# Kernel tuning notes

Hardware: AMD Instinct MI355X
Metric: run time of the kernel (lower is better)

Reference implementation:

```python
import jax, jax.numpy as jnp
import numpy as np

B, NQ, D, NH, L, P = 8, 1000, 256, 8, 4, 4
DFF = 1024
HD = D // NH
SHAPES = np.array([[128, 128], [64, 64], [32, 32], [16, 16]], dtype=np.int64)
S = int((SHAPES[:, 0] * SHAPES[:, 1]).sum())  # 21760
LEVEL_START = np.concatenate([np.zeros(1, np.int64), np.cumsum(SHAPES[:, 0] * SHAPES[:, 1])[:-1]])


def setup_inputs() -> dict:
    key = jax.random.key(0)
    ks = jax.random.split(key, 20)
    w = lambda k, shape, s=0.02: jax.random.normal(k, shape, jnp.float32) * s
    z = lambda n: jnp.zeros((n,), jnp.float32)
    return dict(
        query=w(ks[0], (B, NQ, D), 1.0),
        query_pos=w(ks[1], (B, NQ, D), 1.0),
        reference_points=jax.random.uniform(ks[2], (B, NQ, L, 4), jnp.float32),
        input_flatten=w(ks[3], (B, S, D), 1.0),
        input_spatial_shapes=SHAPES,
        input_level_start_index=LEVEL_START,
        Wq=w(ks[4], (D, D)), bq=z(D), Wk=w(ks[5], (D, D)), bk=z(D),
        Wv=w(ks[6], (D, D)), bv=z(D), Wo=w(ks[7], (D, D)), bo=z(D),
        ln1_g=jnp.ones((D,), jnp.float32), ln1_b=z(D),
        W_off=w(ks[8], (D, NH * L * P * 2)), b_off=z(NH * L * P * 2),
        W_attn=w(ks[9], (D, NH * L * P)), b_attn=z(NH * L * P),
        W_val=w(ks[10], (D, D)), b_val=z(D),
        W_cout=w(ks[11], (D, D)), b_cout=z(D),
        ln2_g=jnp.ones((D,), jnp.float32), ln2_b=z(D),
        W1=w(ks[12], (D, DFF)), b1=z(DFF),
        W2=w(ks[13], (DFF, D)), b2=z(D),
        ln3_g=jnp.ones((D,), jnp.float32), ln3_b=z(D),
    )


def layer_norm(x, g, b, eps=1e-5):
    mu = x.mean(-1, keepdims=True)
    var = ((x - mu) ** 2).mean(-1, keepdims=True)
    return (x - mu) / jnp.sqrt(var + eps) * g + b


def _ms_deform(value, shapes_np, loc, aw):
    # value: (B,S,NH,HD); loc: (B,Nq,NH,L,P,2) in [0,1]; aw: (B,Nq,NH,L,P)
    Bz, _, nh, hd = value.shape
    Nq = loc.shape[1]
    awt = aw.transpose(0, 2, 1, 3, 4)  # (B,NH,Nq,L,P)
    acc = jnp.zeros((Bz, nh, Nq, hd), value.dtype)
    start = 0
    for lvl in range(shapes_np.shape[0]):
        Hl, Wl = int(shapes_np[lvl, 0]), int(shapes_np[lvl, 1])
        vf = value[:, start:start + Hl * Wl].transpose(0, 2, 1, 3)  # (B,NH,Hl*Wl,HD)
        start += Hl * Wl
        # grid_sample align_corners=False: pixel coord = loc * size - 0.5
        lx = loc[:, :, :, lvl, :, 0].transpose(0, 2, 1, 3) * Wl - 0.5  # (B,NH,Nq,P)
        ly = loc[:, :, :, lvl, :, 1].transpose(0, 2, 1, 3) * Hl - 0.5
        x0 = jnp.floor(lx); y0 = jnp.floor(ly)
        tx = lx - x0; ty = ly - y0
        x0i = x0.astype(jnp.int32); y0i = y0.astype(jnp.int32)

        def gather(xi, yi):
            valid = (xi >= 0) & (xi < Wl) & (yi >= 0) & (yi < Hl)
            idx = jnp.clip(yi, 0, Hl - 1) * Wl + jnp.clip(xi, 0, Wl - 1)
            out = jnp.take_along_axis(vf, idx.reshape(Bz, nh, Nq * P)[..., None], axis=2)
            return out.reshape(Bz, nh, Nq, P, hd) * valid[..., None]

        g00 = gather(x0i, y0i)
        g01 = gather(x0i + 1, y0i)
        g10 = gather(x0i, y0i + 1)
        g11 = gather(x0i + 1, y0i + 1)
        samp = (g00 * ((1 - tx) * (1 - ty))[..., None] + g01 * (tx * (1 - ty))[..., None]
                + g10 * ((1 - tx) * ty)[..., None] + g11 * (tx * ty)[..., None])  # (B,NH,Nq,P,HD)
        acc = acc + jnp.einsum('bhqp,bhqpd->bhqd', awt[:, :, :, lvl], samp)
    return acc.transpose(0, 2, 1, 3).reshape(Bz, Nq, nh * hd)


def reference(query, query_pos, reference_points, input_flatten, input_spatial_shapes,
              input_level_start_index, Wq, bq, Wk, bk, Wv, bv, Wo, bo, ln1_g, ln1_b,
              W_off, b_off, W_attn, b_attn, W_val, b_val, W_cout, b_cout, ln2_g, ln2_b,
              W1, b1, W2, b2, ln3_g, ln3_b):
    Bz, Nq, Dm = query.shape
    # --- self-attention (post-norm), pos added to Q/K only ---
    qp = query + query_pos
    q = (qp @ Wq + bq).reshape(Bz, Nq, NH, HD)
    k = (qp @ Wk + bk).reshape(Bz, Nq, NH, HD)
    v = (query @ Wv + bv).reshape(Bz, Nq, NH, HD)
    att = jax.nn.softmax(jnp.einsum('bqhd,bkhd->bhqk', q, k) / jnp.sqrt(jnp.float32(HD)), axis=-1)
    sa = jnp.einsum('bhqk,bkhd->bqhd', att, v).reshape(Bz, Nq, Dm) @ Wo + bo
    x = layer_norm(query + sa, ln1_g, ln1_b)
    # --- deformable cross-attention ---
    q2 = x + query_pos
    value = (input_flatten @ W_val + b_val).reshape(Bz, -1, NH, HD)
    off = (q2 @ W_off + b_off).reshape(Bz, Nq, NH, L, P, 2)
    aw = jax.nn.softmax((q2 @ W_attn + b_attn).reshape(Bz, Nq, NH, L * P), axis=-1)
    aw = aw.reshape(Bz, Nq, NH, L, P)
    rp = reference_points  # (B,Nq,L,4) cxcywh
    loc = rp[:, :, None, :, None, :2] + off / P * rp[:, :, None, :, None, 2:] * 0.5
    shapes_np = np.asarray(input_spatial_shapes)
    ca = _ms_deform(value, shapes_np, loc, aw) @ W_cout + b_cout
    x = layer_norm(x + ca, ln2_g, ln2_b)
    # --- FFN ---
    ffn = jax.nn.relu(x @ W1 + b1) @ W2 + b2
    return layer_norm(x + ffn, ln3_g, ln3_b)
```

## Files before the change

kernel.cpp:

```cpp
#include <hip/hip_runtime.h>
#include <hip/hip_bf16.h>

#define B_   8
#define NQ_  1000
#define D_   256
#define NH_  8
#define L_   4
#define P_   4
#define DFF_ 1024
#define HD_  32
#define S_   21760
#define NTOK (B_*NQ_)

typedef short  bf16x8 __attribute__((ext_vector_type(8)));
typedef float  f32x4  __attribute__((ext_vector_type(4)));

#define WAITBAR(N) asm volatile("s_waitcnt vmcnt(" #N ") lgkmcnt(0)\n\ts_barrier" ::: "memory")
#define ENDBAR()   asm volatile("s_barrier" ::: "memory")

__device__ inline unsigned short f32_to_bf16_bits(float f) {
    unsigned int u = __float_as_uint(f);
    unsigned int rounding = 0x7FFFu + ((u >> 16) & 1u);
    u += rounding;
    return (unsigned short)(u >> 16);
}
__device__ inline float bf16_bits_to_f32(unsigned short b) {
    return __uint_as_float(((unsigned int)b) << 16);
}
__device__ inline unsigned int pack_trunc(float f0, float f1) {
    return __builtin_amdgcn_perm(__float_as_uint(f1), __float_as_uint(f0), 0x07060302u);
}
__device__ inline void async_copy16(const void* g, void* l) {
    __builtin_amdgcn_global_load_lds((const __attribute__((address_space(1))) unsigned int*)g,
                                     (__attribute__((address_space(3))) unsigned int*)l, 16, 0, 0);
}

struct PrepArgs {
    const float* wsrc[10];
    unsigned short* wdst[10];
    int wK[10], wN[10];
    const float* bq; const float* bk; const float* bv; const float* boff; const float* battn;
    float* qkvb; float* oab;
    const float* query; const float* qpos;
    unsigned short* q_bf; unsigned short* qp_bf;
};
__global__ __launch_bounds__(256) void prep_k(PrepArgs P)
{
    const int bid = blockIdx.x, tid = threadIdx.x;
    if (bid < 640) {
        const int job = bid >> 6, tile = bid & 63;
        const int K = P.wK[job], N = P.wN[job];
        const int tilesN = N >> 6;
        if (tile >= (K >> 6) * tilesN) return;
        const int kt = tile / tilesN, nt = tile - kt * tilesN;
        const int k0 = kt * 64, n0 = nt * 64;
        __shared__ unsigned short t_[64][65];
        const float* src = P.wsrc[job];
        unsigned short* dst = P.wdst[job];
        const int cc = tid & 63, rr = tid >> 6;
        #pragma unroll
        for (int i = 0; i < 16; i++) {
            int k = i * 4 + rr;
            t_[k][cc] = f32_to_bf16_bits(src[(size_t)(k0 + k) * N + n0 + cc]);
        }
        __syncthreads();
        #pragma unroll
        for (int i = 0; i < 16; i++) {
            int n = i * 4 + rr;
            dst[(size_t)(n0 + n) * K + k0 + cc] = t_[cc][n];
        }
    } else if (bid == 640) {
        P.qkvb[tid]       = P.bq[tid];
        P.qkvb[256 + tid] = P.bk[tid];
        P.qkvb[512 + tid] = P.bv[tid];
        P.oab[tid]        = P.boff[tid];
        if (tid < 128) P.oab[256 + tid] = P.battn[tid];
    } else {
        const int base = (bid - 641) * 1024 + tid;
        float4 fq[4][2], fp[4][2];
        #pragma unroll
        for (int i = 0; i < 4; i++) {
            const float* q = P.query + (size_t)(base + i * 256) * 8;
            const float* p = P.qpos  + (size_t)(base + i * 256) * 8;
            fq[i][0] = *reinterpret_cast<const float4*>(q);
            fq[i][1] = *reinterpret_cast<const float4*>(q + 4);
            fp[i][0] = *reinterpret_cast<const float4*>(p);
            fp[i][1] = *reinterpret_cast<const float4*>(p + 4);
        }
        #pragma unroll
        for (int i = 0; i < 4; i++) {
            uint4 tq, tp;
            tq.x = pack_trunc(fq[i][0].x, fq[i][0].y);
            tq.y = pack_trunc(fq[i][0].z, fq[i][0].w);
            tq.z = pack_trunc(fq[i][1].x, fq[i][1].y);
            tq.w = pack_trunc(fq[i][1].z, fq[i][1].w);
            tp.x = pack_trunc(fq[i][0].x + fp[i][0].x, fq[i][0].y + fp[i][0].y);
            tp.y = pack_trunc(fq[i][0].z + fp[i][0].z, fq[i][0].w + fp[i][0].w);
            tp.z = pack_trunc(fq[i][1].x + fp[i][1].x, fq[i][1].y + fp[i][1].y);
            tp.w = pack_trunc(fq[i][1].z + fp[i][1].z, fq[i][1].w + fp[i][1].w);
            *reinterpret_cast<uint4*>(P.q_bf  + (size_t)(base + i * 256) * 8) = tq;
            *reinterpret_cast<uint4*>(P.qp_bf + (size_t)(base + i * 256) * 8) = tp;
        }
    }
}

__global__ __launch_bounds__(256) void vgemmF(const float* __restrict__ Af,
                                              const unsigned short* __restrict__ Bt,
                                              const float* __restrict__ bias,
                                              unsigned short* __restrict__ Cb)
{
    constexpr int K = 256;
    constexpr int N = 256;
    __shared__ __align__(16) float          sA[2][128 * 32];
    __shared__ __align__(16) unsigned short sB[2][128 * 32];
    const int tid = threadIdx.x;
    const int w = tid >> 6, l = tid & 63;
    const int n0 = blockIdx.x * 128, m0 = blockIdx.y * 128;
    const int wr = w >> 1, wc = w & 1;
    const int lq = l & 15, g = l >> 4;

    f32x4 acc[4][4];
    #pragma unroll
    for (int i = 0; i < 4; i++)
        #pragma unroll
        for (int j = 0; j < 4; j++)
            #pragma unroll
            for (int r = 0; r < 4; r++) acc[i][j][r] = 0.f;

    auto issueA = [&](int t, int buf) {
        #pragma unroll
        for (int r = 0; r < 4; r++) {
            int lin = (r * 256 + tid) * 16;
            int row = lin >> 7;
            int kb  = (lin & 127) ^ ((row & 7) << 4);
            async_copy16(Af + (size_t)(m0 + row) * K + t * 32 + (kb >> 2),
                         (char*)sA[buf] + lin);
        }
    };
    auto issueB = [&](int t, int buf) {
        #pragma unroll
        for (int r = 0; r < 2; r++) {
            int lin = (r * 256 + tid) * 16;
            int row = lin >> 6;
            int kb  = (lin & 63) ^ ((row & 3) << 4);
            async_copy16(Bt + (size_t)(n0 + row) * K + t * 32 + (kb >> 1),
                         (char*)sB[buf] + lin);
        }
    };

    issueA(0, 0);
    issueB(0, 0);

    for (int t = 0; t < 8; t++) {
        const int cur = t & 1;
        if (t + 1 < 8) {
            issueA(t + 1, cur ^ 1);
            issueB(t + 1, cur ^ 1);
            WAITBAR(6);
        } else {
            WAITBAR(0);
        }

        bf16x8 afr[4], bfr[4];
        #pragma unroll
        for (int mi = 0; mi < 4; mi++) {
            int row = wr * 64 + mi * 16 + lq;
            int sw  = (row & 7) << 4;
            int p0  = (g * 32) ^ sw;
            const char* p = (const char*)sA[cur] + row * 128;
            float4 a0 = *reinterpret_cast<const float4*>(p + p0);
            float4 a1 = *reinterpret_cast<const float4*>(p + (p0 ^ 16));
            uint4 u;
            u.x = pack_trunc(a0.x, a0.y);
            u.y = pack_trunc(a0.z, a0.w);
            u.z = pack_trunc(a1.x, a1.y);
            u.w = pack_trunc(a1.z, a1.w);
            afr[mi] = *reinterpret_cast<bf16x8*>(&u);
        }
        #pragma unroll
        for (int ni = 0; ni < 4; ni++) {
            int row = wc * 64 + ni * 16 + lq;
            int off = (g * 16) ^ ((row & 3) << 4);
            bfr[ni] = *reinterpret_cast<const bf16x8*>((const char*)sB[cur] + row * 64 + off);
        }
        #pragma unroll
        for (int mi = 0; mi < 4; mi++)
            #pragma unroll
            for (int ni = 0; ni < 4; ni++)
                acc[mi][ni] = __builtin_amdgcn_mfma_f32_16x16x32_bf16(
                    afr[mi], bfr[ni], acc[mi][ni], 0, 0, 0);
        ENDBAR();
    }

    #pragma unroll
    for (int mi = 0; mi < 4; mi++) {
        #pragma unroll
        for (int ni = 0; ni < 4; ni++) {
            int col = n0 + wc * 64 + ni * 16 + lq;
            float bz = bias[col];
            #pragma unroll
            for (int rg = 0; rg < 4; rg++) {
                int row = m0 + wr * 64 + mi * 16 + g * 4 + rg;
                Cb[(size_t)row * N + col] = f32_to_bf16_bits(acc[mi][ni][rg] + bz);
            }
        }
    }
}

__global__ __launch_bounds__(256) void qkv_gemm(const unsigned short* __restrict__ qp_bf,
                                                const unsigned short* __restrict__ q_bf,
                                                const unsigned short* __restrict__ Bt,
                                                const float* __restrict__ bias,
                                                unsigned short* __restrict__ qk_out,
                                                unsigned short* __restrict__ vt_out)
{
    constexpr int K = 256;
    constexpr int BN = 64;
    __shared__ __align__(16) unsigned short sB[BN * K];

    const int tid = threadIdx.x;
    const int w = tid >> 6, l = tid & 63;
    const int g = l >> 4, lr = l & 15;
    const int n0 = blockIdx.x * BN;
    const bool isV = (n0 >= 512);
    const unsigned short* Ab = isV ? q_bf : qp_bf;

    #pragma unroll
    for (int r = 0; r < 8; r++) {
        int lin = (r * 256 + tid) * 16;
        int row = lin >> 9;
        int kb  = (lin & 511) ^ ((row & 7) << 4);
        async_copy16(Bt + (size_t)(n0 + row) * K + (kb >> 1), (char*)sB + lin);
    }
    asm volatile("s_waitcnt vmcnt(0)\n\ts_barrier" ::: "memory");

    float bz[4];
    #pragma unroll
    for (int nf = 0; nf < 4; nf++) bz[nf] = bias[n0 + nf * 16 + lr];

    const int m0w = blockIdx.y * 64 + w * 16;
    const int arow = m0w + lr;

    f32x4 acc[4];
    #pragma unroll
    for (int nf = 0; nf < 4; nf++)
        #pragma unroll
        for (int r = 0; r < 4; r++) acc[nf][r] = 0.f;

    #pragma unroll
    for (int kf = 0; kf < 8; kf++) {
        bf16x8 af = *reinterpret_cast<const bf16x8*>(Ab + (size_t)arow * K + kf * 32 + g * 8);
        #pragma unroll
        for (int nf = 0; nf < 4; nf++) {
            int brow = nf * 16 + lr;
            bf16x8 bf = *reinterpret_cast<const bf16x8*>(
                (const char*)sB + brow * 512 + ((kf * 64 + g * 16) ^ ((brow & 7) << 4)));
            acc[nf] = __builtin_amdgcn_mfma_f32_16x16x32_bf16(af, bf, acc[nf], 0, 0, 0);
        }
    }

    if (!isV) {
        #pragma unroll
        for (int nf = 0; nf < 4; nf++) {
            int col = n0 + nf * 16 + lr;
            #pragma unroll
            for (int rg = 0; rg < 4; rg++) {
                int row = m0w + g * 4 + rg;
                qk_out[(size_t)row * 512 + col] = f32_to_bf16_bits(acc[nf][rg] + bz[nf]);
            }
        }
    } else {
        #pragma unroll
        for (int nf = 0; nf < 4; nf++) {
            int col = n0 - 512 + nf * 16 + lr;
            int row0 = m0w + g * 4;
            int bb = row0 / 1000;
            int key = row0 - bb * 1000;
            ushort4 q4;
            q4.x = f32_to_bf16_bits(acc[nf][0] + bz[nf]);
            q4.y = f32_to_bf16_bits(acc[nf][1] + bz[nf]);
            q4.z = f32_to_bf16_bits(acc[nf][2] + bz[nf]);
            q4.w = f32_to_bf16_bits(acc[nf][3] + bz[nf]);
            *reinterpret_cast<ushort4*>(vt_out + (size_t)bb * 262144 + (size_t)col * 1024 + key) = q4;
        }
    }
}

template<bool RELU, int CMODE, int BN, int K>
__global__ __launch_bounds__(256) void bgemm(const unsigned short* __restrict__ Ab,
                                             const unsigned short* __restrict__ Bt,
                                             const float* __restrict__ bias,
                                             float* __restrict__ Cf,
                                             unsigned short* __restrict__ Cb,
                                             int N)
{
    constexpr int NF   = BN / 16;
    constexpr int KF   = K / 32;
    constexpr int ROWB = K * 2;
    constexpr int FILL = BN * ROWB / 4096;

    __shared__ __align__(16) unsigned short sB[BN * K];

    const int tid = threadIdx.x;
    const int w = tid >> 6, l = tid & 63;
    const int g = l >> 4, lr = l & 15;
    const int n0 = blockIdx.x * BN;

    #pragma unroll
    for (int r = 0; r < FILL; r++) {
        int lin = (r * 256 + tid) * 16;
        int row = lin / ROWB;
        int kb  = (lin & (ROWB - 1)) ^ ((row & 7) << 4);
        async_copy16(Bt + (size_t)(n0 + row) * K + (kb >> 1), (char*)sB + lin);
    }
    asm volatile("s_waitcnt vmcnt(0)\n\ts_barrier" ::: "memory");

    float bz[NF];
    #pragma unroll
    for (int nf = 0; nf < NF; nf++) bz[nf] = bias[n0 + nf * 16 + lr];

    const int m0w = blockIdx.y * 64 + w * 16;
    const int arow = m0w + lr;

    f32x4 acc[NF];
    #pragma unroll
    for (int nf = 0; nf < NF; nf++)
        #pragma unroll
        for (int r = 0; r < 4; r++) acc[nf][r] = 0.f;

    #pragma unroll
    for (int kf = 0; kf < KF; kf++) {
        bf16x8 af = *reinterpret_cast<const bf16x8*>(Ab + (size_t)arow * K + kf * 32 + g * 8);
        #pragma unroll
        for (int nf = 0; nf < NF; nf++) {
            int brow = nf * 16 + lr;
            bf16x8 bf = *reinterpret_cast<const bf16x8*>(
                (const char*)sB + brow * ROWB + ((kf * 64 + g * 16) ^ ((brow & 7) << 4)));
            acc[nf] = __builtin_amdgcn_mfma_f32_16x16x32_bf16(af, bf, acc[nf], 0, 0, 0);
        }
    }

    #pragma unroll
    for (int nf = 0; nf < NF; nf++) {
        int col = n0 + nf * 16 + lr;
        #pragma unroll
        for (int rg = 0; rg < 4; rg++) {
            int row = m0w + g * 4 + rg;
            float v = acc[nf][rg] + bz[nf];
            if (RELU) v = fmaxf(v, 0.f);
            if constexpr (CMODE == 1)
                Cb[(size_t)row * N + col] = f32_to_bf16_bits(v);
            else
                Cf[(size_t)row * N + col] = v;
        }
    }
}

__global__ __launch_bounds__(256) void fattn_k(const unsigned short* __restrict__ qk,
                                               const unsigned short* __restrict__ vt,
                                               unsigned short* __restrict__ sa)
{
    const int b = blockIdx.z, h = blockIdx.y;
    const int tid = threadIdx.x;
    const int w = tid >> 6, l = tid & 63;
    const int lq = l & 15, g = l >> 4;
    const int q0 = blockIdx.x * 64 + w * 16;

    __shared__ __align__(16) unsigned short Ks[2][128 * 32];
    __shared__ __align__(16) unsigned short Vs[2][32 * 128];
    __shared__ __align__(16) unsigned short Ps[4][16 * 128];

    int qrow = q0 + lq; if (qrow > NQ_ - 1) qrow = NQ_ - 1;
    const bf16x8 qfrag = *reinterpret_cast<const bf16x8*>(
        qk + ((size_t)(b * NQ_ + qrow)) * 512 + h * 32 + g * 8);

    f32x4 O0 = {0.f, 0.f, 0.f, 0.f}, O1 = {0.f, 0.f, 0.f, 0.f};
    float m = -1e30f, lsum = 0.f;
    const float scale = 0.17677669529663687f;

    const size_t kbase = (size_t)b * (NQ_ * 512) + 256 + h * 32;
    const size_t vbase = (size_t)b * 262144 + (size_t)(h * 32) * 1024;
    const int swz = (lq & 7) << 4;

    auto issueKV = [&](int kt, int buf) {
        #pragma unroll
        for (int r = 0; r < 2; r++) {
            int lin = (r * 256 + tid) * 16;
            int krow = lin >> 6;
            int kb = (lin & 63) ^ ((krow & 7) << 4);
            async_copy16(qk + kbase + (size_t)(kt * 128 + krow) * 512 + (kb >> 1),
                         (char*)Ks[buf] + lin);
            int d = lin >> 8;
            int vb = (lin & 255) ^ ((d & 7) << 4);
            async_copy16(vt + vbase + (size_t)d * 1024 + kt * 128 + (vb >> 1),
                         (char*)Vs[buf] + lin);
        }
    };

    issueKV(0, 0);

    for (int kt = 0; kt < 8; kt++) {
        const int k0 = kt * 128;
        const int cur = kt & 1;
        asm volatile("s_waitcnt vmcnt(0) lgkmcnt(0)\n\ts_barrier" ::: "memory");
        if (kt < 7) issueKV(kt + 1, cur ^ 1);

        const unsigned short* Kc = Ks[cur];
        const unsigned short* Vc = Vs[cur];

        float t[8][4];
        float tmax = -1e30f;
        const bool tail = (k0 + 128 > NQ_);
        #pragma unroll
        for (int ni = 0; ni < 8; ni++) {
            int row = ni * 16 + lq;
            bf16x8 kf = *reinterpret_cast<const bf16x8*>(
                (const char*)Kc + row * 64 + ((g * 16) ^ swz));
            f32x4 st = __builtin_amdgcn_mfma_f32_16x16x32_bf16(
                kf, qfrag, (f32x4){0.f, 0.f, 0.f, 0.f}, 0, 0, 0);
            #pragma unroll
            for (int rg = 0; rg < 4; rg++) {
                float tv = st[rg] * scale;
                if (tail) {
                    int key = k0 + ni * 16 + g * 4 + rg;
                    tv = (key < NQ_) ? tv : -1e30f;
                }
                t[ni][rg] = tv;
                tmax = fmaxf(tmax, tv);
            }
        }
        tmax = fmaxf(tmax, __shfl_xor(tmax, 16));
        tmax = fmaxf(tmax, __shfl_xor(tmax, 32));
        float mnew = fmaxf(m, tmax);
        float corr = __expf(m - mnew);
        m = mnew;

        float rs = 0.f;
        unsigned int pk[8][2];
        #pragma unroll
        for (int ni = 0; ni < 8; ni++) {
            float p0 = __expf(t[ni][0] - mnew);
            float p1 = __expf(t[ni][1] - mnew);
            float p2 = __expf(t[ni][2] - mnew);
            float p3 = __expf(t[ni][3] - mnew);
            rs += (p0 + p1) + (p2 + p3);
            pk[ni][0] = ((unsigned)f32_to_bf16_bits(p0)) | (((unsigned)f32_to_bf16_bits(p1)) << 16);
            pk[ni][1] = ((unsigned)f32_to_bf16_bits(p2)) | (((unsigned)f32_to_bf16_bits(p3)) << 16);
        }
        rs += __shfl_xor(rs, 16);
        rs += __shfl_xor(rs, 32);
        lsum = lsum * corr + rs;

        float c0 = __shfl(corr, g * 4 + 0);
        float c1 = __shfl(corr, g * 4 + 1);
        float c2 = __shfl(corr, g * 4 + 2);
        float c3 = __shfl(corr, g * 4 + 3);
        O0[0] *= c0; O0[1] *= c1; O0[2] *= c2; O0[3] *= c3;
        O1[0] *= c0; O1[1] *= c1; O1[2] *= c2; O1[3] *= c3;

        unsigned short* Pw = Ps[w];
        #pragma unroll
        for (int ni = 0; ni < 8; ni++) {
            int byteoff = lq * 256 + ((ni * 32 + g * 8) ^ swz);
            *reinterpret_cast<uint2*>((char*)Pw + byteoff) = make_uint2(pk[ni][0], pk[ni][1]);
        }

        #pragma unroll
        for (int c = 0; c < 4; c++) {
            int rb = (c * 64 + g * 16) ^ swz;
            bf16x8 pa = *reinterpret_cast<const bf16x8*>((const char*)Pw + lq * 256 + rb);
            bf16x8 v0 = *reinterpret_cast<const bf16x8*>((const char*)Vc + lq * 256 + rb);
            bf16x8 v1 = *reinterpret_cast<const bf16x8*>((const char*)Vc + (16 + lq) * 256 + rb);
            O0 = __builtin_amdgcn_mfma_f32_16x16x32_bf16(pa, v0, O0, 0, 0, 0);
            O1 = __builtin_amdgcn_mfma_f32_16x16x32_bf16(pa, v1, O1, 0, 0, 0);
        }
    }

    float linv = 1.f / lsum;
    float i0 = __shfl(linv, g * 4 + 0);
    float i1 = __shfl(linv, g * 4 + 1);
    float i2 = __shfl(linv, g * 4 + 2);
    float i3 = __shfl(linv, g * 4 + 3);
    float iv[4] = {i0, i1, i2, i3};
    #pragma unroll
    for (int rg = 0; rg < 4; rg++) {
        int qg = q0 + g * 4 + rg;
        if (qg < NQ_) {
            size_t obase = ((size_t)(b * NQ_ + qg)) * 256 + h * 32;
            sa[obase + lq]      = f32_to_bf16_bits(O0[rg] * iv[rg]);
            sa[obase + 16 + lq] = f32_to_bf16_bits(O1[rg] * iv[rg]);
        }
    }
}

template<int OM>
__global__ __launch_bounds__(256) void ln_k(const float* __restrict__ a,
                                            const float* __restrict__ bsum,
                                            const float* __restrict__ pos,
                                            const float* __restrict__ g,
                                            const float* __restrict__ be,
                                            float* __restrict__ out,
                                            unsigned short* __restrict__ outb)
{
    const int wave = threadIdx.x >> 6, lane = threadIdx.x & 63;
    const int row = blockIdx.x * 4 + wave;
    float4 xa = reinterpret_cast<const float4*>(a + (size_t)row * 256)[lane];
    float4 xb = reinterpret_cast<const float4*>(bsum + (size_t)row * 256)[lane];
    float4 x = {xa.x + xb.x, xa.y + xb.y, xa.z + xb.z, xa.w + xb.w};
    float s  = x.x + x.y + x.z + x.w;
    float ss = x.x * x.x + x.y * x.y + x.z * x.z + x.w * x.w;
    #pragma unroll
    for (int off = 32; off > 0; off >>= 1) {
        s  += __shfl_xor(s, off);
        ss += __shfl_xor(ss, off);
    }
    float mu  = s * (1.f / 256.f);
    float var = ss * (1.f / 256.f) - mu * mu;
    float rstd = rsqrtf(var + 1e-5f);
    float4 gv = reinterpret_cast<const float4*>(g)[lane];
    float4 bv = reinterpret_cast<const float4*>(be)[lane];
    float4 o = {(x.x - mu) * rstd * gv.x + bv.x,
                (x.y - mu) * rstd * gv.y + bv.y,
                (x.z - mu) * rstd * gv.z + bv.z,
                (x.w - mu) * rstd * gv.w + bv.w};
    reinterpret_cast<float4*>(out + (size_t)row * 256)[lane] = o;
    if constexpr (OM == 1) {
        ushort4 q4;
        q4.x = f32_to_bf16_bits(o.x); q4.y = f32_to_bf16_bits(o.y);
        q4.z = f32_to_bf16_bits(o.z); q4.w = f32_to_bf16_bits(o.w);
        *reinterpret_cast<ushort4*>(outb + (size_t)row * 256 + lane * 4) = q4;
    } else if constexpr (OM == 2) {
        float4 pv = reinterpret_cast<const float4*>(pos + (size_t)row * 256)[lane];
        ushort4 q4;
        q4.x = f32_to_bf16_bits(o.x + pv.x); q4.y = f32_to_bf16_bits(o.y + pv.y);
        q4.z = f32_to_bf16_bits(o.z + pv.z); q4.w = f32_to_bf16_bits(o.w + pv.w);
        *reinterpret_cast<ushort4*>(outb + (size_t)row * 256 + lane * 4) = q4;
    }
}

__device__ inline unsigned int samp2(const unsigned short* __restrict__ v,
                                     int b, int st, int Wl, int Hl,
                                     int x, int y, int hc)
{
    bool valid = (x >= 0) & (x < Wl) & (y >= 0) & (y < Hl);
    int xc = min(max(x, 0), Wl - 1);
    int yc = min(max(y, 0), Hl - 1);
    size_t idx = ((size_t)(b * S_ + st + yc * Wl + xc)) * 256 + hc;
    unsigned int val = *reinterpret_cast<const unsigned int*>(v + idx);
    return valid ? val : 0u;
}

__global__ __launch_bounds__(256) void deform_k(const float* __restrict__ rp,
                                                const float* __restrict__ oa,
                                                const unsigned short* __restrict__ value,
                                                unsigned short* __restrict__ ca)
{
    const int tk = threadIdx.x >> 7;
    const int tok = blockIdx.x * 2 + tk;
    const int b = tok / NQ_;
    const int h = (threadIdx.x >> 4) & 7;
    const int cp = threadIdx.x & 15;
    const int hc = h * 32 + cp * 2;

    const float* awp = oa + (size_t)tok * 384 + 256 + h * 16;
    float w[16];
    float mx = -1e30f;
    #pragma unroll
    for (int i = 0; i < 16; i++) { w[i] = awp[i]; mx = fmaxf(mx, w[i]); }
    float sum = 0.f;
    #pragma unroll
    for (int i = 0; i < 16; i++) { w[i] = __expf(w[i] - mx); sum += w[i]; }
    const float inv = 1.f / sum;

    const float* rpp  = rp + (size_t)tok * (L_ * 4);
    const float* offp = oa + (size_t)tok * 384 + h * 32;

    const int lvlW[4] = {128, 64, 32, 16};
    const int lvlS[4] = {0, 16384, 20480, 21504};

    float acc0 = 0.f, acc1 = 0.f;
    #pragma unroll
    for (int l = 0; l < 4; l++) {
        const int Wl = lvlW[l], Hl = lvlW[l], st = lvlS[l];
        const float cx = rpp[l * 4 + 0], cy = rpp[l * 4 + 1];
        const float cw = rpp[l * 4 + 2], chh = rpp[l * 4 + 3];
        #pragma unroll
        for (int p = 0; p < 4; p++) {
            float ox = offp[l * 8 + p * 2 + 0];
            float oy = offp[l * 8 + p * 2 + 1];
            float lx = (cx + ox * 0.25f * cw * 0.5f) * Wl - 0.5f;
            float ly = (cy + oy * 0.25f * chh * 0.5f) * Hl - 0.5f;
            float x0f = floorf(lx), y0f = floorf(ly);
            float tx = lx - x0f, ty = ly - y0f;
            int x0 = (int)x0f, y0 = (int)y0f;
            unsigned int u00 = samp2(value, b, st, Wl, Hl, x0,     y0,     hc);
            unsigned int u01 = samp2(value, b, st, Wl, Hl, x0 + 1, y0,     hc);
            unsigned int u10 = samp2(value, b, st, Wl, Hl, x0,     y0 + 1, hc);
            unsigned int u11 = samp2(value, b, st, Wl, Hl, x0 + 1, y0 + 1, hc);
            float w00 = (1.f - tx) * (1.f - ty), w01 = tx * (1.f - ty);
            float w10 = (1.f - tx) * ty,         w11 = tx * ty;
            float g0 = bf16_bits_to_f32((unsigned short)u00) * w00
                     + bf16_bits_to_f32((unsigned short)u01) * w01
                     + bf16_bits_to_f32((unsigned short)u10) * w10
                     + bf16_bits_to_f32((unsigned short)u11) * w11;
            float g1 = bf16_bits_to_f32((unsigned short)(u00 >> 16)) * w00
                     + bf16_bits_to_f32((unsigned short)(u01 >> 16)) * w01
                     + bf16_bits_to_f32((unsigned short)(u10 >> 16)) * w10
                     + bf16_bits_to_f32((unsigned short)(u11 >> 16)) * w11;
            float wa = w[l * 4 + p] * inv;
            acc0 += wa * g0;
            acc1 += wa * g1;
        }
    }
    unsigned int packed = ((unsigned)f32_to_bf16_bits(acc0)) | (((unsigned)f32_to_bf16_bits(acc1)) << 16);
    *reinterpret_cast<unsigned int*>(ca + (size_t)tok * 256 + hc) = packed;
}

extern "C" void kernel_launch(void* const* d_in, const int* in_sizes, int n_in,
                              void* d_out, int out_size, void* d_ws, size_t ws_size,
                              hipStream_t stream)
{
    const float* query      = (const float*)d_in[0];
    const float* query_pos  = (const float*)d_in[1];
    const float* ref_pts    = (const float*)d_in[2];
    const float* input_flat = (const float*)d_in[3];
    const float* Wq = (const float*)d_in[6];  const float* bq = (const float*)d_in[7];
    const float* Wk = (const float*)d_in[8];  const float* bk = (const float*)d_in[9];
    const float* Wv = (const float*)d_in[10]; const float* bv = (const float*)d_in[11];
    const float* Wo = (const float*)d_in[12]; const float* bo = (const float*)d_in[13];
    const float* ln1g = (const float*)d_in[14]; const float* ln1b = (const float*)d_in[15];
    const float* W_off = (const float*)d_in[16]; const float* b_off = (const float*)d_in[17];
    const float* W_attn = (const float*)d_in[18]; const float* b_attn = (const float*)d_in[19];
    const float* W_val = (const float*)d_in[20]; const float* b_val = (const float*)d_in[21];
    const float* W_cout = (const float*)d_in[22]; const float* b_cout = (const float*)d_in[23];
    const float* ln2g = (const float*)d_in[24]; const float* ln2b = (const float*)d_in[25];
    const float* W1 = (const float*)d_in[26]; const float* b1 = (const float*)d_in[27];
    const float* W2 = (const float*)d_in[28]; const float* b2 = (const float*)d_in[29];
    const float* ln3g = (const float*)d_in[30]; const float* ln3b = (const float*)d_in[31];
    float* out = (float*)d_out;

    char* base = (char*)d_ws;
    size_t off = 0;
    auto alloc = [&](size_t bytes) { void* p = base + off; off += (bytes + 255) & ~(size_t)255; return p; };
    unsigned short* value_bf = (unsigned short*)alloc((size_t)B_ * S_ * 256 * 2);
    unsigned short* qk_bf = (unsigned short*)alloc((size_t)NTOK * 1024 * 2);
    unsigned short* h_bf = qk_bf;
    unsigned short* vt = (unsigned short*)alloc((size_t)B_ * 256 * 1024 * 2);
    float* oa_buf = (float*)alloc((size_t)NTOK * 384 * 4);
    float* tmp0   = (float*)alloc((size_t)NTOK * 256 * 4);
    float* x1     = (float*)alloc((size_t)NTOK * 256 * 4);
    float* x2     = (float*)alloc((size_t)NTOK * 256 * 4);
    unsigned short* sc_bf  = (unsigned short*)alloc((size_t)NTOK * 256 * 2);
    unsigned short* q_bf   = (unsigned short*)alloc((size_t)NTOK * 256 * 2);
    unsigned short* qp_bf  = (unsigned short*)alloc((size_t)NTOK * 256 * 2);
    unsigned short* x1p_bf = (unsigned short*)alloc((size_t)NTOK * 256 * 2);
    unsigned short* x2_bf  = (unsigned short*)alloc((size_t)NTOK * 256 * 2);
    unsigned short* wqkv  = (unsigned short*)alloc(768 * 256 * 2);
    unsigned short* wo    = (unsigned short*)alloc(256 * 256 * 2);
    unsigned short* woa   = (unsigned short*)alloc(384 * 256 * 2);
    unsigned short* wval  = (unsigned short*)alloc(256 * 256 * 2);
    unsigned short* wcout = (unsigned short*)alloc(256 * 256 * 2);
    unsigned short* w1t   = (unsigned short*)alloc(1024 * 256 * 2);
    unsigned short* w2t   = (unsigned short*)alloc(256 * 1024 * 2);
    float* qkvbias = (float*)alloc(768 * 4);
    float* oabias  = (float*)alloc(384 * 4);

    dim3 blk(256);

    PrepArgs P;
    P.wsrc[0] = Wq;    P.wdst[0] = wqkv;              P.wK[0] = 256;  P.wN[0] = 256;
    P.wsrc[1] = Wk;    P.wdst[1] = wqkv + 256 * 256;  P.wK[1] = 256;  P.wN[1] = 256;
    P.wsrc[2] = Wv;    P.wdst[2] = wqkv + 512 * 256;  P.wK[2] = 256;  P.wN[2] = 256;
    P.wsrc[3] = Wo;    P.wdst[3] = wo;                P.wK[3] = 256;  P.wN[3] = 256;
    P.wsrc[4] = W_off; P.wdst[4] = woa;               P.wK[4] = 256;  P.wN[4] = 256;
    P.wsrc[5] = W_attn;P.wdst[5] = woa + 256 * 256;   P.wK[5] = 256;  P.wN[5] = 128;
    P.wsrc[6] = W_val; P.wdst[6] = wval;              P.wK[6] = 256;  P.wN[6] = 256;
    P.wsrc[7] = W_cout;P.wdst[7] = wcout;             P.wK[7] = 256;  P.wN[7] = 256;
    P.wsrc[8] = W1;    P.wdst[8] = w1t;               P.wK[8] = 256;  P.wN[8] = 1024;
    P.wsrc[9] = W2;    P.wdst[9] = w2t;               P.wK[9] = 1024; P.wN[9] = 256;
    P.bq = bq; P.bk = bk; P.bv = bv; P.boff = b_off; P.battn = b_attn;
    P.qkvb = qkvbias; P.oab = oabias;
    P.query = query; P.qpos = query_pos; P.q_bf = q_bf; P.qp_bf = qp_bf;
    prep_k<<<891, blk, 0, stream>>>(P);

    qkv_gemm<<<dim3(12, 125), blk, 0, stream>>>(qp_bf, q_bf, wqkv, qkvbias, qk_bf, vt);
    fattn_k<<<dim3(16, NH_, B_), blk, 0, stream>>>(qk_bf, vt, sc_bf);
    bgemm<false, 0,  64, 256><<<dim3(4, 125), blk, 0, stream>>>(sc_bf, wo, bo, tmp0, nullptr, 256);
    ln_k<2><<<NTOK / 4, blk, 0, stream>>>(query, tmp0, query_pos, ln1g, ln1b, x1, x1p_bf);

    vgemmF<<<dim3(2, 1360), blk, 0, stream>>>(input_flat, wval, b_val, value_bf);
    bgemm<false, 0,  64, 256><<<dim3(6, 125), blk, 0, stream>>>(x1p_bf, woa, oabias, oa_buf, nullptr, 384);
    deform_k<<<NTOK / 2, blk, 0, stream>>>(ref_pts, oa_buf, value_bf, sc_bf);
    bgemm<false, 0,  64, 256><<<dim3(4, 125), blk, 0, stream>>>(sc_bf, wcout, b_cout, tmp0, nullptr, 256);
    ln_k<1><<<NTOK / 4, blk, 0, stream>>>(x1, tmp0, nullptr, ln2g, ln2b, x2, x2_bf);

    bgemm<true,  1,  64, 256><<<dim3(16, 125), blk, 0, stream>>>(x2_bf, w1t, b1, nullptr, h_bf, 1024);
    bgemm<false, 0,  32, 1024><<<dim3(8, 125), blk, 0, stream>>>(h_bf, w2t, b2, tmp0, nullptr, 256);
    ln_k<0><<<NTOK / 4, blk, 0, stream>>>(x2, tmp0, nullptr, ln3g, ln3b, out, nullptr);
}
```

Baseline: 252.4 us.

## Interleave value-projection GEMM tiles into the self-attention stage kernels

The standalone value-projection GEMM (2720 tiles over input_flatten) is split into four chunks and appended as extra blocks to the QKV, flash-attention, output-projection and first layernorm kernels. These stages are small or latency-bound, so the value GEMM blocks can fill idle compute units alongside them. All four host kernels now declare a 48KB shared buffer so the value-GEMM body fits, which may lower occupancy for the lighter stages such as the layernorm and the Wo GEMM.

```diff
diff --git a/kernel.cpp b/kernel.cpp
--- a/kernel.cpp
+++ b/kernel.cpp
@@ -33,6 +33,116 @@
 __device__ inline void async_copy16(const void* g, void* l) {
     __builtin_amdgcn_global_load_lds((const __attribute__((address_space(1))) unsigned int*)g,
                                      (__attribute__((address_space(3))) unsigned int*)l, 16, 0, 0);
+}
+
+struct VArgs {
+    const float* Af;
+    const unsigned short* Bt;
+    const float* bias;
+    unsigned short* Cb;
+};
+
+__device__ inline void vgemm_body(char* smem, int vbid, const VArgs V)
+{
+    constexpr int K = 256;
+    constexpr int N = 256;
+    float* sA0 = reinterpret_cast<float*>(smem);
+    unsigned short* sB0 = reinterpret_cast<unsigned short*>(smem + 32768);
+
+    const int tid = threadIdx.x;
+    const int w = tid >> 6, l = tid & 63;
+    const int n0 = (vbid & 1) * 128, m0 = (vbid >> 1) * 128;
+    const int wr = w >> 1, wc = w & 1;
+    const int lq = l & 15, g = l >> 4;
+
+    f32x4 acc[4][4];
+    #pragma unroll
+    for (int i = 0; i < 4; i++)
+        #pragma unroll
+        for (int j = 0; j < 4; j++)
+            #pragma unroll
+            for (int r = 0; r < 4; r++) acc[i][j][r] = 0.f;
+
+    auto issueA = [&](int t, int buf) {
+        #pragma unroll
+        for (int r = 0; r < 4; r++) {
+            int lin = (r * 256 + tid) * 16;
+            int row = lin >> 7;
+            int kb  = (lin & 127) ^ ((row & 7) << 4);
+            async_copy16(V.Af + (size_t)(m0 + row) * K + t * 32 + (kb >> 2),
+                         (char*)(sA0 + (size_t)buf * 4096) + lin);
+        }
+    };
+    auto issueB = [&](int t, int buf) {
+        #pragma unroll
+        for (int r = 0; r < 2; r++) {
+            int lin = (r * 256 + tid) * 16;
+            int row = lin >> 6;
+            int kb  = (lin & 63) ^ ((row & 3) << 4);
+            async_copy16(V.Bt + (size_t)(n0 + row) * K + t * 32 + (kb >> 1),
+                         (char*)(sB0 + (size_t)buf * 4096) + lin);
+        }
+    };
+
+    issueA(0, 0);
+    issueB(0, 0);
+
+    for (int t = 0; t < 8; t++) {
+        const int cur = t & 1;
+        if (t + 1 < 8) {
+            issueA(t + 1, cur ^ 1);
+            issueB(t + 1, cur ^ 1);
+            WAITBAR(6);
+        } else {
+            WAITBAR(0);
+        }
+
+        const float* sA = sA0 + (size_t)cur * 4096;
+        const unsigned short* sB = sB0 + (size_t)cur * 4096;
+        bf16x8 afr[4], bfr[4];
+        #pragma unroll
+        for (int mi = 0; mi < 4; mi++) {
+            int row = wr * 64 + mi * 16 + lq;
+            int sw  = (row & 7) << 4;
+            int p0  = (g * 32) ^ sw;
+            const char* p = (const char*)sA + row * 128;
+            float4 a0 = *reinterpret_cast<const float4*>(p + p0);
+            float4 a1 = *reinterpret_cast<const float4*>(p + (p0 ^ 16));
+            uint4 u;
+            u.x = pack_trunc(a0.x, a0.y);
+            u.y = pack_trunc(a0.z, a0.w);
+            u.z = pack_trunc(a1.x, a1.y);
+            u.w = pack_trunc(a1.z, a1.w);
+            afr[mi] = *reinterpret_cast<bf16x8*>(&u);
+        }
+        #pragma unroll
+        for (int ni = 0; ni < 4; ni++) {
+            int row = wc * 64 + ni * 16 + lq;
+            int off = (g * 16) ^ ((row & 3) << 4);
+            bfr[ni] = *reinterpret_cast<const bf16x8*>((const char*)sB + row * 64 + off);
+        }
+        #pragma unroll
+        for (int mi = 0; mi < 4; mi++)
+            #pragma unroll
+            for (int ni = 0; ni < 4; ni++)
+                acc[mi][ni] = __builtin_amdgcn_mfma_f32_16x16x32_bf16(
+                    afr[mi], bfr[ni], acc[mi][ni], 0, 0, 0);
+        ENDBAR();
+    }
+
+    #pragma unroll
+    for (int mi = 0; mi < 4; mi++) {
+        #pragma unroll
+        for (int ni = 0; ni < 4; ni++) {
+            int col = n0 + wc * 64 + ni * 16 + lq;
+            float bz = V.bias[col];
+            #pragma unroll
+            for (int rg = 0; rg < 4; rg++) {
+                int row = m0 + wr * 64 + mi * 16 + g * 4 + rg;
+                V.Cb[(size_t)row * N + col] = f32_to_bf16_bits(acc[mi][ni][rg] + bz);
+            }
+        }
+    }
 }
 
 struct PrepArgs {
@@ -104,124 +214,26 @@
     }
 }
 
-__global__ __launch_bounds__(256) void vgemmF(const float* __restrict__ Af,
-                                              const unsigned short* __restrict__ Bt,
-                                              const float* __restrict__ bias,
-                                              unsigned short* __restrict__ Cb)
-{
+__global__ __launch_bounds__(256) void qkvF(const unsigned short* __restrict__ qp_bf,
+                                            const unsigned short* __restrict__ q_bf,
+                                            const unsigned short* __restrict__ Bt,
+                                            const float* __restrict__ bias,
+                                            unsigned short* __restrict__ qk_out,
+                                            unsigned short* __restrict__ vt_out,
+                                            VArgs V)
+{
+    __shared__ __align__(16) char smem[49152];
+    const int bid = blockIdx.x;
+    if (bid >= 1500) { vgemm_body(smem, bid - 1500, V); return; }
+
     constexpr int K = 256;
-    constexpr int N = 256;
-    __shared__ __align__(16) float          sA[2][128 * 32];
-    __shared__ __align__(16) unsigned short sB[2][128 * 32];
-    const int tid = threadIdx.x;
-    const int w = tid >> 6, l = tid & 63;
-    const int n0 = blockIdx.x * 128, m0 = blockIdx.y * 128;
-    const int wr = w >> 1, wc = w & 1;
-    const int lq = l & 15, g = l >> 4;
-
-    f32x4 acc[4][4];
-    #pragma unroll
-    for (int i = 0; i < 4; i++)
-        #pragma unroll
-        for (int j = 0; j < 4; j++)
-            #pragma unroll
-            for (int r = 0; r < 4; r++) acc[i][j][r] = 0.f;
-
-    auto issueA = [&](int t, int buf) {
-        #pragma unroll
-        for (int r = 0; r < 4; r++) {
-            int lin = (r * 256 + tid) * 16;
-            int row = lin >> 7;
-            int kb  = (lin & 127) ^ ((row & 7) << 4);
-            async_copy16(Af + (size_t)(m0 + row) * K + t * 32 + (kb >> 2),
-                         (char*)sA[buf] + lin);
-        }
-    };
-    auto issueB = [&](int t, int buf) {
-        #pragma unroll
-        for (int r = 0; r < 2; r++) {
-            int lin = (r * 256 + tid) * 16;
-            int row = lin >> 6;
-            int kb  = (lin & 63) ^ ((row & 3) << 4);
-            async_copy16(Bt + (size_t)(n0 + row) * K + t * 32 + (kb >> 1),
-                         (char*)sB[buf] + lin);
-        }
-    };
-
-    issueA(0, 0);
-    issueB(0, 0);
-
-    for (int t = 0; t < 8; t++) {
-        const int cur = t & 1;
-        if (t + 1 < 8) {
-            issueA(t + 1, cur ^ 1);
-            issueB(t + 1, cur ^ 1);
-            WAITBAR(6);
-        } else {
-            WAITBAR(0);
-        }
-
-        bf16x8 afr[4], bfr[4];
-        #pragma unroll
-        for (int mi = 0; mi < 4; mi++) {
-            int row = wr * 64 + mi * 16 + lq;
-            int sw  = (row & 7) << 4;
-            int p0  = (g * 32) ^ sw;
-            const char* p = (const char*)sA[cur] + row * 128;
-            float4 a0 = *reinterpret_cast<const float4*>(p + p0);
-            float4 a1 = *reinterpret_cast<const float4*>(p + (p0 ^ 16));
-            uint4 u;
-            u.x = pack_trunc(a0.x, a0.y);
-            u.y = pack_trunc(a0.z, a0.w);
-            u.z = pack_trunc(a1.x, a1.y);
-            u.w = pack_trunc(a1.z, a1.w);
-            afr[mi] = *reinterpret_cast<bf16x8*>(&u);
-        }
-        #pragma unroll
-        for (int ni = 0; ni < 4; ni++) {
-            int row = wc * 64 + ni * 16 + lq;
-            int off = (g * 16) ^ ((row & 3) << 4);
-            bfr[ni] = *reinterpret_cast<const bf16x8*>((const char*)sB[cur] + row * 64 + off);
-        }
-        #pragma unroll
-        for (int mi = 0; mi < 4; mi++)
-            #pragma unroll
-            for (int ni = 0; ni < 4; ni++)
-                acc[mi][ni] = __builtin_amdgcn_mfma_f32_16x16x32_bf16(
-                    afr[mi], bfr[ni], acc[mi][ni], 0, 0, 0);
-        ENDBAR();
-    }
-
-    #pragma unroll
-    for (int mi = 0; mi < 4; mi++) {
-        #pragma unroll
-        for (int ni = 0; ni < 4; ni++) {
-            int col = n0 + wc * 64 + ni * 16 + lq;
-            float bz = bias[col];
-            #pragma unroll
-            for (int rg = 0; rg < 4; rg++) {
-                int row = m0 + wr * 64 + mi * 16 + g * 4 + rg;
-                Cb[(size_t)row * N + col] = f32_to_bf16_bits(acc[mi][ni][rg] + bz);
-            }
-        }
-    }
-}
-
-__global__ __launch_bounds__(256) void qkv_gemm(const unsigned short* __restrict__ qp_bf,
-                                                const unsigned short* __restrict__ q_bf,
-                                                const unsigned short* __restrict__ Bt,
-                                                const float* __restrict__ bias,
-                                                unsigned short* __restrict__ qk_out,
-                                                unsigned short* __restrict__ vt_out)
-{
-    constexpr int K = 256;
-    constexpr int BN = 64;
-    __shared__ __align__(16) unsigned short sB[BN * K];
+    unsigned short* sB = reinterpret_cast<unsigned short*>(smem);
 
     const int tid = threadIdx.x;
     const int w = tid >> 6, l = tid & 63;
     const int g = l >> 4, lr = l & 15;
-    const int n0 = blockIdx.x * BN;
+    const int n0 = (bid % 12) * 64;
+    const int my = bid / 12;
     const bool isV = (n0 >= 512);
     const unsigned short* Ab = isV ? q_bf : qp_bf;
 
@@ -238,7 +250,7 @@
     #pragma unroll
     for (int nf = 0; nf < 4; nf++) bz[nf] = bias[n0 + nf * 16 + lr];
 
-    const int m0w = blockIdx.y * 64 + w * 16;
+    const int m0w = my * 64 + w * 16;
     const int arow = m0w + lr;
 
     f32x4 acc[4];
@@ -286,89 +298,24 @@
     }
 }
 
-template<bool RELU, int CMODE, int BN, int K>
-__global__ __launch_bounds__(256) void bgemm(const unsigned short* __restrict__ Ab,
-                                             const unsigned short* __restrict__ Bt,
-                                             const float* __restrict__ bias,
-                                             float* __restrict__ Cf,
-                                             unsigned short* __restrict__ Cb,
-                                             int N)
-{
-    constexpr int NF   = BN / 16;
-    constexpr int KF   = K / 32;
-    constexpr int ROWB = K * 2;
-    constexpr int FILL = BN * ROWB / 4096;
-
-    __shared__ __align__(16) unsigned short sB[BN * K];
-
-    const int tid = threadIdx.x;
-    const int w = tid >> 6, l = tid & 63;
-    const int g = l >> 4, lr = l & 15;
-    const int n0 = blockIdx.x * BN;
-
-    #pragma unroll
-    for (int r = 0; r < FILL; r++) {
-        int lin = (r * 256 + tid) * 16;
-        int row = lin / ROWB;
-        int kb  = (lin & (ROWB - 1)) ^ ((row & 7) << 4);
-        async_copy16(Bt + (size_t)(n0 + row) * K + (kb >> 1), (char*)sB + lin);
-    }
-    asm volatile("s_waitcnt vmcnt(0)\n\ts_barrier" ::: "memory");
-
-    float bz[NF];
-    #pragma unroll
-    for (int nf = 0; nf < NF; nf++) bz[nf] = bias[n0 + nf * 16 + lr];
-
-    const int m0w = blockIdx.y * 64 + w * 16;
-    const int arow = m0w + lr;
-
-    f32x4 acc[NF];
-    #pragma unroll
-    for (int nf = 0; nf < NF; nf++)
-        #pragma unroll
-        for (int r = 0; r < 4; r++) acc[nf][r] = 0.f;
-
-    #pragma unroll
-    for (int kf = 0; kf < KF; kf++) {
-        bf16x8 af = *reinterpret_cast<const bf16x8*>(Ab + (size_t)arow * K + kf * 32 + g * 8);
-        #pragma unroll
-        for (int nf = 0; nf < NF; nf++) {
-            int brow = nf * 16 + lr;
-            bf16x8 bf = *reinterpret_cast<const bf16x8*>(
-                (const char*)sB + brow * ROWB + ((kf * 64 + g * 16) ^ ((brow & 7) << 4)));
-            acc[nf] = __builtin_amdgcn_mfma_f32_16x16x32_bf16(af, bf, acc[nf], 0, 0, 0);
-        }
-    }
-
-    #pragma unroll
-    for (int nf = 0; nf < NF; nf++) {
-        int col = n0 + nf * 16 + lr;
-        #pragma unroll
-        for (int rg = 0; rg < 4; rg++) {
-            int row = m0w + g * 4 + rg;
-            float v = acc[nf][rg] + bz[nf];
-            if (RELU) v = fmaxf(v, 0.f);
-            if constexpr (CMODE == 1)
-                Cb[(size_t)row * N + col] = f32_to_bf16_bits(v);
-            else
-                Cf[(size_t)row * N + col] = v;
-        }
-    }
-}
-
-__global__ __launch_bounds__(256) void fattn_k(const unsigned short* __restrict__ qk,
-                                               const unsigned short* __restrict__ vt,
-                                               unsigned short* __restrict__ sa)
-{
-    const int b = blockIdx.z, h = blockIdx.y;
+__global__ __launch_bounds__(256) void fattnF(const unsigned short* __restrict__ qk,
+                                              const unsigned short* __restrict__ vt,
+                                              unsigned short* __restrict__ sa,
+                                              VArgs V)
+{
+    __shared__ __align__(16) char smem[49152];
+    const int bid = blockIdx.x;
+    if (bid >= 1024) { vgemm_body(smem, 654 + bid - 1024, V); return; }
+
+    unsigned short* Ks0 = reinterpret_cast<unsigned short*>(smem);
+    unsigned short* Vs0 = reinterpret_cast<unsigned short*>(smem + 16384);
+    unsigned short* Ps  = reinterpret_cast<unsigned short*>(smem + 32768);
+
+    const int b = bid >> 7, h = (bid >> 4) & 7;
     const int tid = threadIdx.x;
     const int w = tid >> 6, l = tid & 63;
     const int lq = l & 15, g = l >> 4;
-    const int q0 = blockIdx.x * 64 + w * 16;
-
-    __shared__ __align__(16) unsigned short Ks[2][128 * 32];
-    __shared__ __align__(16) unsigned short Vs[2][32 * 128];
-    __shared__ __align__(16) unsigned short Ps[4][16 * 128];
+    const int q0 = (bid & 15) * 64 + w * 16;
 
     int qrow = q0 + lq; if (qrow > NQ_ - 1) qrow = NQ_ - 1;
     const bf16x8 qfrag = *reinterpret_cast<const bf16x8*>(
@@ -389,11 +336,11 @@
             int krow = lin >> 6;
             int kb = (lin & 63) ^ ((krow & 7) << 4);
             async_copy16(qk + kbase + (size_t)(kt * 128 + krow) * 512 + (kb >> 1),
-                         (char*)Ks[buf] + lin);
+                         (char*)(Ks0 + (size_t)buf * 4096) + lin);
             int d = lin >> 8;
             int vb = (lin & 255) ^ ((d & 7) << 4);
             async_copy16(vt + vbase + (size_t)d * 1024 + kt * 128 + (vb >> 1),
-                         (char*)Vs[buf] + lin);
+                         (char*)(Vs0 + (size_t)buf * 4096) + lin);
         }
     };
 
@@ -405,8 +352,8 @@
         asm volatile("s_waitcnt vmcnt(0) lgkmcnt(0)\n\ts_barrier" ::: "memory");
         if (kt < 7) issueKV(kt + 1, cur ^ 1);
 
-        const unsigned short* Kc = Ks[cur];
-        const unsigned short* Vc = Vs[cur];
+        const unsigned short* Kc = Ks0 + (size_t)cur * 4096;
+        const unsigned short* Vc = Vs0 + (size_t)cur * 4096;
 
         float t[8][4];
         float tmax = -1e30f;
@@ -458,7 +405,7 @@
         O0[0] *= c0; O0[1] *= c1; O0[2] *= c2; O0[3] *= c3;
         O1[0] *= c0; O1[1] *= c1; O1[2] *= c2; O1[3] *= c3;
 
-        unsigned short* Pw = Ps[w];
+        unsigned short* Pw = Ps + (size_t)w * 2048;
         #pragma unroll
         for (int ni = 0; ni < 8; ni++) {
             int byteoff = lq * 256 + ((ni * 32 + g * 8) ^ swz);
@@ -493,10 +440,185 @@
     }
 }
 
+__global__ __launch_bounds__(256) void woF(const unsigned short* __restrict__ Ab,
+                                           const unsigned short* __restrict__ Bt,
+                                           const float* __restrict__ bias,
+                                           float* __restrict__ Cf,
+                                           VArgs V)
+{
+    __shared__ __align__(16) char smem[49152];
+    const int bid = blockIdx.x;
+    if (bid >= 500) { vgemm_body(smem, 1700 + bid - 500, V); return; }
+
+    constexpr int K = 256;
+    unsigned short* sB = reinterpret_cast<unsigned short*>(smem);
+
+    const int tid = threadIdx.x;
+    const int w = tid >> 6, l = tid & 63;
+    const int g = l >> 4, lr = l & 15;
+    const int n0 = (bid & 3) * 64;
+    const int my = bid >> 2;
+
+    #pragma unroll
+    for (int r = 0; r < 8; r++) {
+        int lin = (r * 256 + tid) * 16;
+        int row = lin >> 9;
+        int kb  = (lin & 511) ^ ((row & 7) << 4);
+        async_copy16(Bt + (size_t)(n0 + row) * K + (kb >> 1), (char*)sB + lin);
+    }
+    asm volatile("s_waitcnt vmcnt(0)\n\ts_barrier" ::: "memory");
+
+    float bz[4];
+    #pragma unroll
+    for (int nf = 0; nf < 4; nf++) bz[nf] = bias[n0 + nf * 16 + lr];
+
+    const int m0w = my * 64 + w * 16;
+    const int arow = m0w + lr;
+
+    f32x4 acc[4];
+    #pragma unroll
+    for (int nf = 0; nf < 4; nf++)
+        #pragma unroll
+        for (int r = 0; r < 4; r++) acc[nf][r] = 0.f;
+
+    #pragma unroll
+    for (int kf = 0; kf < 8; kf++) {
+        bf16x8 af = *reinterpret_cast<const bf16x8*>(Ab + (size_t)arow * K + kf * 32 + g * 8);
+        #pragma unroll
+        for (int nf = 0; nf < 4; nf++) {
+            int brow = nf * 16 + lr;
+            bf16x8 bf = *reinterpret_cast<const bf16x8*>(
+                (const char*)sB + brow * 512 + ((kf * 64 + g * 16) ^ ((brow & 7) << 4)));
+            acc[nf] = __builtin_amdgcn_mfma_f32_16x16x32_bf16(af, bf, acc[nf], 0, 0, 0);
+        }
+    }
+
+    #pragma unroll
+    for (int nf = 0; nf < 4; nf++) {
+        int col = n0 + nf * 16 + lr;
+        #pragma unroll
+        for (int rg = 0; rg < 4; rg++) {
+            int row = m0w + g * 4 + rg;
+            Cf[(size_t)row * 256 + col] = acc[nf][rg] + bz[nf];
+        }
+    }
+}
+
+__global__ __launch_bounds__(256) void ln1F(const float* __restrict__ a,
+                                            const float* __restrict__ bsum,
+                                            const float* __restrict__ pos,
+                                            const float* __restrict__ g,
+                                            const float* __restrict__ be,
+                                            float* __restrict__ out,
+                                            unsigned short* __restrict__ outb,
+                                            VArgs V)
+{
+    __shared__ __align__(16) char smem[49152];
+    const int bid = blockIdx.x;
+    if (bid >= 2000) { vgemm_body(smem, 2223 + bid - 2000, V); return; }
+
+    const int wave = threadIdx.x >> 6, lane = threadIdx.x & 63;
+    const int row = bid * 4 + wave;
+    float4 xa = reinterpret_cast<const float4*>(a + (size_t)row * 256)[lane];
+    float4 xb = reinterpret_cast<const float4*>(bsum + (size_t)row * 256)[lane];
+    float4 x = {xa.x + xb.x, xa.y + xb.y, xa.z + xb.z, xa.w + xb.w};
+    float s  = x.x + x.y + x.z + x.w;
+    float ss = x.x * x.x + x.y * x.y + x.z * x.z + x.w * x.w;
+    #pragma unroll
+    for (int off = 32; off > 0; off >>= 1) {
+        s  += __shfl_xor(s, off);
+        ss += __shfl_xor(ss, off);
+    }
+    float mu  = s * (1.f / 256.f);
+    float var = ss * (1.f / 256.f) - mu * mu;
+    float rstd = rsqrtf(var + 1e-5f);
+    float4 gv = reinterpret_cast<const float4*>(g)[lane];
+    float4 bv = reinterpret_cast<const float4*>(be)[lane];
+    float4 o = {(x.x - mu) * rstd * gv.x + bv.x,
+                (x.y - mu) * rstd * gv.y + bv.y,
+                (x.z - mu) * rstd * gv.z + bv.z,
+                (x.w - mu) * rstd * gv.w + bv.w};
+    reinterpret_cast<float4*>(out + (size_t)row * 256)[lane] = o;
+    float4 pv = reinterpret_cast<const float4*>(pos + (size_t)row * 256)[lane];
+    ushort4 q4;
+    q4.x = f32_to_bf16_bits(o.x + pv.x); q4.y = f32_to_bf16_bits(o.y + pv.y);
+    q4.z = f32_to_bf16_bits(o.z + pv.z); q4.w = f32_to_bf16_bits(o.w + pv.w);
+    *reinterpret_cast<ushort4*>(outb + (size_t)row * 256 + lane * 4) = q4;
+}
+
+template<bool RELU, int CMODE, int BN, int K>
+__global__ __launch_bounds__(256) void bgemm(const unsigned short* __restrict__ Ab,
+                                             const unsigned short* __restrict__ Bt,
+                                             const float* __restrict__ bias,
+                                             float* __restrict__ Cf,
+                                             unsigned short* __restrict__ Cb,
+                                             int N)
+{
+    constexpr int NF   = BN / 16;
+    constexpr int KF   = K / 32;
+    constexpr int ROWB = K * 2;
+    constexpr int FILL = BN * ROWB / 4096;
+
+    __shared__ __align__(16) unsigned short sB[BN * K];
+
+    const int tid = threadIdx.x;
+    const int w = tid >> 6, l = tid & 63;
+    const int g = l >> 4, lr = l & 15;
+    const int n0 = blockIdx.x * BN;
+
+    #pragma unroll
+    for (int r = 0; r < FILL; r++) {
+        int lin = (r * 256 + tid) * 16;
+        int row = lin / ROWB;
+        int kb  = (lin & (ROWB - 1)) ^ ((row & 7) << 4);
+        async_copy16(Bt + (size_t)(n0 + row) * K + (kb >> 1), (char*)sB + lin);
+    }
+    asm volatile("s_waitcnt vmcnt(0)\n\ts_barrier" ::: "memory");
+
+    float bz[NF];
+    #pragma unroll
+    for (int nf = 0; nf < NF; nf++) bz[nf] = bias[n0 + nf * 16 + lr];
+
+    const int m0w = blockIdx.y * 64 + w * 16;
+    const int arow = m0w + lr;
+
+    f32x4 acc[NF];
+    #pragma unroll
+    for (int nf = 0; nf < NF; nf++)
+        #pragma unroll
+        for (int r = 0; r < 4; r++) acc[nf][r] = 0.f;
+
+    #pragma unroll
+    for (int kf = 0; kf < KF; kf++) {
+        bf16x8 af = *reinterpret_cast<const bf16x8*>(Ab + (size_t)arow * K + kf * 32 + g * 8);
+        #pragma unroll
+        for (int nf = 0; nf < NF; nf++) {
+            int brow = nf * 16 + lr;
+            bf16x8 bf = *reinterpret_cast<const bf16x8*>(
+                (const char*)sB + brow * ROWB + ((kf * 64 + g * 16) ^ ((brow & 7) << 4)));
+            acc[nf] = __builtin_amdgcn_mfma_f32_16x16x32_bf16(af, bf, acc[nf], 0, 0, 0);
+        }
+    }
+
+    #pragma unroll
+    for (int nf = 0; nf < NF; nf++) {
+        int col = n0 + nf * 16 + lr;
+        #pragma unroll
+        for (int rg = 0; rg < 4; rg++) {
+            int row = m0w + g * 4 + rg;
+            float v = acc[nf][rg] + bz[nf];
+            if (RELU) v = fmaxf(v, 0.f);
+            if constexpr (CMODE == 1)
+                Cb[(size_t)row * N + col] = f32_to_bf16_bits(v);
+            else
+                Cf[(size_t)row * N + col] = v;
+        }
+    }
+}
+
 template<int OM>
 __global__ __launch_bounds__(256) void ln_k(const float* __restrict__ a,
                                             const float* __restrict__ bsum,
-                                            const float* __restrict__ pos,
                                             const float* __restrict__ g,
                                             const float* __restrict__ be,
                                             float* __restrict__ out,
@@ -528,12 +650,6 @@
         ushort4 q4;
         q4.x = f32_to_bf16_bits(o.x); q4.y = f32_to_bf16_bits(o.y);
         q4.z = f32_to_bf16_bits(o.z); q4.w = f32_to_bf16_bits(o.w);
-        *reinterpret_cast<ushort4*>(outb + (size_t)row * 256 + lane * 4) = q4;
-    } else if constexpr (OM == 2) {
-        float4 pv = reinterpret_cast<const float4*>(pos + (size_t)row * 256)[lane];
-        ushort4 q4;
-        q4.x = f32_to_bf16_bits(o.x + pv.x); q4.y = f32_to_bf16_bits(o.y + pv.y);
-        q4.z = f32_to_bf16_bits(o.z + pv.z); q4.w = f32_to_bf16_bits(o.w + pv.w);
         *reinterpret_cast<ushort4*>(outb + (size_t)row * 256 + lane * 4) = q4;
     }
 }
@@ -683,18 +799,20 @@
     P.query = query; P.qpos = query_pos; P.q_bf = q_bf; P.qp_bf = qp_bf;
     prep_k<<<891, blk, 0, stream>>>(P);
 
-    qkv_gemm<<<dim3(12, 125), blk, 0, stream>>>(qp_bf, q_bf, wqkv, qkvbias, qk_bf, vt);
-    fattn_k<<<dim3(16, NH_, B_), blk, 0, stream>>>(qk_bf, vt, sc_bf);
-    bgemm<false, 0,  64, 256><<<dim3(4, 125), blk, 0, stream>>>(sc_bf, wo, bo, tmp0, nullptr, 256);
-    ln_k<2><<<NTOK / 4, blk, 0, stream>>>(query, tmp0, query_pos, ln1g, ln1b, x1, x1p_bf);
-
-    vgemmF<<<dim3(2, 1360), blk, 0, stream>>>(input_flat, wval, b_val, value_bf);
+    VArgs V;
+    V.Af = input_flat; V.Bt = wval; V.bias = b_val; V.Cb = value_bf;
+
+    qkvF <<<1500 + 654,  blk, 0, stream>>>(qp_bf, q_bf, wqkv, qkvbias, qk_bf, vt, V);
+    fattnF<<<1024 + 1046, blk, 0, stream>>>(qk_bf, vt, sc_bf, V);
+    woF  <<<500 + 523,   blk, 0, stream>>>(sc_bf, wo, bo, tmp0, V);
+    ln1F <<<2000 + 497,  blk, 0, stream>>>(query, tmp0, query_pos, ln1g, ln1b, x1, x1p_bf, V);
+
     bgemm<false, 0,  64, 256><<<dim3(6, 125), blk, 0, stream>>>(x1p_bf, woa, oabias, oa_buf, nullptr, 384);
     deform_k<<<NTOK / 2, blk, 0, stream>>>(ref_pts, oa_buf, value_bf, sc_bf);
     bgemm<false, 0,  64, 256><<<dim3(4, 125), blk, 0, stream>>>(sc_bf, wcout, b_cout, tmp0, nullptr, 256);
-    ln_k<1><<<NTOK / 4, blk, 0, stream>>>(x1, tmp0, nullptr, ln2g, ln2b, x2, x2_bf);
+    ln_k<1><<<NTOK / 4, blk, 0, stream>>>(x1, tmp0, ln2g, ln2b, x2, x2_bf);
 
     bgemm<true,  1,  64, 256><<<dim3(16, 125), blk, 0, stream>>>(x2_bf, w1t, b1, nullptr, h_bf, 1024);
     bgemm<false, 0,  32, 1024><<<dim3(8, 125), blk, 0, stream>>>(h_bf, w2t, b2, tmp0, nullptr, 256);
-    ln_k<0><<<NTOK / 4, blk, 0, stream>>>(x2, tmp0, nullptr, ln3g, ln3b, out, nullptr);
-}
+    ln_k<0><<<NTOK / 4, blk, 0, stream>>>(x2, tmp0, ln3g, ln3b, out, nullptr);
+}
```

Measured after the change: 337.6 us. 1.34x slower.
